# Performance work log

Measured on AMD Instinct MI355X. Metric: run time of the kernel, lower is better.

## Reference

```python
import jax, jax.numpy as jnp
import numpy as np

MIN_PERSISTENCE = [0.0, 0.0]  # from init kwargs, one per homology dimension


def setup_inputs() -> dict:
    key = jax.random.key(0)
    k1, k2, k3 = jax.random.split(key, 3)
    D = 512
    N = D * D * D  # 134,217,728 voxels
    P = 2_000_000  # persistence pairs per homology dimension
    X = jax.random.normal(k1, (D, D, D), dtype=jnp.float32)
    # Stand-ins for GUDHI cofaces_of_persistence_pairs() output:
    # flat (birth_idx, death_idx) pairs into Xflat, interleaved, per dimension.
    indices0 = jax.random.randint(k2, (2 * P,), 0, N, dtype=jnp.int32)
    indices1 = jax.random.randint(k3, (2 * P,), 0, N, dtype=jnp.int32)
    return {"X": X, "indices0": indices0, "indices1": indices1}


def _diagram(Xflat, indices, min_pers):
    # gather birth/death filtration values -> [num_pairs, 2]
    dgm = jnp.take(Xflat, indices).reshape(-1, 2)
    if min_pers >= 0:
        # Original uses tf.where + gather (dynamic shape). For jit we keep a
        # fixed shape and zero out points with persistence <= min_pers.
        keep = jnp.abs(dgm[:, 1] - dgm[:, 0]) > min_pers
        dgm = jnp.where(keep[:, None], dgm, jnp.zeros((), dgm.dtype))
    return dgm


def reference(X, indices0, indices1):
    Xflat = X.reshape(-1)
    dgm0 = _diagram(Xflat, indices0, MIN_PERSISTENCE[0])
    dgm1 = _diagram(Xflat, indices1, MIN_PERSISTENCE[1])
    return (dgm0, dgm1)
```

## Files before the change

### kernel.cpp

```cpp
#include <hip/hip_runtime.h>
#include <hip/hip_bf16.h>


__global__ __launch_bounds__(256) void gather_diagram_kernel(
    const float* __restrict__ Xflat,
    const int* __restrict__ idx,
    float* __restrict__ out,
    int P) {
    int p = blockIdx.x * blockDim.x + threadIdx.x;
    if (p >= P) return;
    int2 ij = reinterpret_cast<const int2*>(idx)[p];
    float b = Xflat[ij.x];
    float d = Xflat[ij.y];
    bool keep = fabsf(d - b) > 0.0f;
    float2 o;
    o.x = keep ? b : 0.0f;
    o.y = keep ? d : 0.0f;
    reinterpret_cast<float2*>(out)[p] = o;
}

extern "C" void kernel_launch(void* const* d_in, const int* in_sizes, int n_in,
                              void* d_out, int out_size, void* d_ws, size_t ws_size,
                              hipStream_t stream) {
    const float* X        = (const float*)d_in[0];
    const int*   indices0 = (const int*)d_in[1];
    const int*   indices1 = (const int*)d_in[2];
    float*       out      = (float*)d_out;

    const int P0 = in_sizes[1] / 2;
    const int P1 = in_sizes[2] / 2;

    const int block = 256;
    gather_diagram_kernel<<<(P0 + block - 1) / block, block, 0, stream>>>(
        X, indices0, out, P0);
    gather_diagram_kernel<<<(P1 + block - 1) / block, block, 0, stream>>>(
        X, indices1, out + (size_t)P0 * 2, P1);
}
```

Measured before the change: 751.9 us.

## Merge both gathers into one launch with vectorized nontemporal loads and stores

Replaces the two per-dimension launches with a single kernel. Each thread handles four 16-byte chunks, so it processes two pairs per chunk and issues 16 independent random gathers, which raises memory-level parallelism. Index reads and output writes use 128-bit nontemporal accesses so streaming data does not pollute the cache that serves the random gathers into X. The persistence test becomes a `!=` comparison. This differs from `fabs(d-b) > 0` when both values are infinite or NaN. The code also assumes the index counts are multiples of four.

Result: no change. 748.5 us (-0.5%).

```diff
diff --git a/kernel.cpp b/kernel.cpp
--- a/kernel.cpp
+++ b/kernel.cpp
@@ -2,21 +2,56 @@
 #include <hip/hip_bf16.h>
 
 
+typedef int   v4i __attribute__((ext_vector_type(4)));
+typedef float v4f __attribute__((ext_vector_type(4)));
+
 __global__ __launch_bounds__(256) void gather_diagram_kernel(
-    const float* __restrict__ Xflat,
-    const int* __restrict__ idx,
+    const float* __restrict__ X,
+    const int* __restrict__ idx0,
+    const int* __restrict__ idx1,
     float* __restrict__ out,
-    int P) {
-    int p = blockIdx.x * blockDim.x + threadIdx.x;
-    if (p >= P) return;
-    int2 ij = reinterpret_cast<const int2*>(idx)[p];
-    float b = Xflat[ij.x];
-    float d = Xflat[ij.y];
-    bool keep = fabsf(d - b) > 0.0f;
-    float2 o;
-    o.x = keep ? b : 0.0f;
-    o.y = keep ? d : 0.0f;
-    reinterpret_cast<float2*>(out)[p] = o;
+    int n4_0,
+    int n4_total)
+{
+    constexpr int C = 4;
+    const int tid    = blockIdx.x * blockDim.x + threadIdx.x;
+    const int stride = gridDim.x * blockDim.x;
+
+    int  c[C];
+    v4i  ij[C];
+    bool ok[C];
+    #pragma unroll
+    for (int j = 0; j < C; ++j) {
+        c[j]  = tid + j * stride;
+        ok[j] = c[j] < n4_total;
+        int cc = ok[j] ? c[j] : 0;
+        const v4i* p = (cc < n4_0)
+            ? reinterpret_cast<const v4i*>(idx0) + cc
+            : reinterpret_cast<const v4i*>(idx1) + (cc - n4_0);
+        ij[j] = __builtin_nontemporal_load(p);
+    }
+
+    float v[C][4];
+    #pragma unroll
+    for (int j = 0; j < C; ++j) {
+        v[j][0] = X[ij[j].x];
+        v[j][1] = X[ij[j].y];
+        v[j][2] = X[ij[j].z];
+        v[j][3] = X[ij[j].w];
+    }
+
+    #pragma unroll
+    for (int j = 0; j < C; ++j) {
+        bool k0 = v[j][1] != v[j][0];
+        bool k1 = v[j][3] != v[j][2];
+        v4f o;
+        o.x = k0 ? v[j][0] : 0.0f;
+        o.y = k0 ? v[j][1] : 0.0f;
+        o.z = k1 ? v[j][2] : 0.0f;
+        o.w = k1 ? v[j][3] : 0.0f;
+        if (ok[j])
+            __builtin_nontemporal_store(o, reinterpret_cast<v4f*>(out) + c[j]);
+    }
 }
 
 extern "C" void kernel_launch(void* const* d_in, const int* in_sizes, int n_in,
@@ -27,12 +62,13 @@
     const int*   indices1 = (const int*)d_in[2];
     float*       out      = (float*)d_out;
 
-    const int P0 = in_sizes[1] / 2;
-    const int P1 = in_sizes[2] / 2;
+    const int n4_0     = in_sizes[1] / 4;
+    const int n4_total = (in_sizes[1] + in_sizes[2]) / 4;
 
-    const int block = 256;
-    gather_diagram_kernel<<<(P0 + block - 1) / block, block, 0, stream>>>(
-        X, indices0, out, P0);
-    gather_diagram_kernel<<<(P1 + block - 1) / block, block, 0, stream>>>(
-        X, indices1, out + (size_t)P0 * 2, P1);
+    constexpr int C = 4, BLOCK = 256;
+    const int threads_needed = (n4_total + C - 1) / C;
+    const int blocks = (threads_needed + BLOCK - 1) / BLOCK;
+
+    gather_diagram_kernel<<<blocks, BLOCK, 0, stream>>>(
+        X, indices0, indices1, out, n4_0, n4_total);
 }
```
